# Optimization experiments

Measured on AMD Instinct MI355X. Metric: run time of the kernel, lower is better.

Reference implementation:

```python
import jax, jax.numpy as jnp
import numpy as np


def setup_inputs() -> dict:
    key = jax.random.key(0)
    k1, k2, k3 = jax.random.split(key, 3)
    B, T, J, D = 32, 1024, 128, 256  # D = 2 * input_dim
    ctx_embd = jax.random.normal(k1, (B, T, D), dtype=jnp.float32)
    query_embd = jax.random.normal(k2, (B, J, D), dtype=jnp.float32)
    # nn.Linear(6*input_dim, 1, bias=False) weight flattened: [w1 | w2 | w3], each of size D
    w = jax.random.normal(k3, (3 * D,), dtype=jnp.float32) * (1.0 / np.sqrt(3 * D))
    return {"ctx_embd": ctx_embd, "query_embd": query_embd, "w": w}


def reference(ctx_embd, query_embd, w):
    D = ctx_embd.shape[-1]
    w1, w2, w3 = w[:D], w[D:2 * D], w[2 * D:]
    # Trilinear score S[b,t,j] = ctx.w1 + query.w2 + (ctx*query).w3, decomposed
    # (algebraically identical to Linear(cat(ctx, query, ctx*query))).
    s_ctx = ctx_embd @ w1            # [B, T]
    s_qry = query_embd @ w2          # [B, J]
    s_mul = jnp.einsum('btd,bjd->btj', ctx_embd * w3, query_embd)  # [B, T, J]
    S = s_ctx[:, :, None] + s_qry[:, None, :] + s_mul              # [B, T, J]
    # Context-to-query attention
    a = jax.nn.softmax(S, axis=-1)                                 # [B, T, J]
    c2q = jnp.einsum('btj,bjd->btd', a, query_embd)                # [B, T, D]
    # Query-to-context attention
    b = jax.nn.softmax(jnp.max(S, axis=2), axis=-1)                # [B, T]
    q2c = jnp.einsum('bt,btd->bd', b, ctx_embd)[:, None, :]        # [B, 1, D] broadcast over T
    G = jnp.concatenate(
        [ctx_embd, c2q, ctx_embd * c2q, ctx_embd * q2c], axis=-1)  # [B, T, 4D]
    return G
```

## Files before the change

kernel.cpp:

```cpp
#include <hip/hip_runtime.h>

typedef float f4 __attribute__((ext_vector_type(4)));
typedef short s8v __attribute__((ext_vector_type(8)));
typedef unsigned int u2v __attribute__((ext_vector_type(2)));
typedef unsigned int u4v __attribute__((ext_vector_type(4)));

#define B_ 32
#define T_ 1024
#define J_ 128
#define D_ 256

__device__ inline unsigned short f2bf(float x) {
    unsigned int u = __float_as_uint(x);
    u += 0x7fffu + ((u >> 16) & 1u);
    return (unsigned short)(u >> 16);
}

__device__ __forceinline__ void ldsload16(const void* g, void* l) {
    __builtin_amdgcn_global_load_lds(
        (const __attribute__((address_space(1))) void*)g,
        (__attribute__((address_space(3))) void*)l, 16, 0, 0);
}

__global__ __launch_bounds__(256) void k_pre(const float* __restrict__ q, const float* __restrict__ w,
                                             unsigned short* __restrict__ Bqh, float* __restrict__ sq,
                                             unsigned short* __restrict__ qTh) {
    __shared__ float t_[16][260];
    int b = blockIdx.x >> 3, jt = blockIdx.x & 7;
    int tid = threadIdx.x;
    const float* qb = q + (b * J_ + jt * 16) * D_;

#pragma unroll
    for (int k = 0; k < 4; k++) {
        int idx = tid + (k << 8);
        int jj = idx >> 6, d4 = idx & 63;
        f4 v = *(const f4*)(qb + jj * D_ + (d4 << 2));
        *(f4*)&t_[jj][d4 << 2] = v;
        f4 w1v = *(const f4*)(w + (d4 << 2));
        f4 w3v = *(const f4*)(w + 2 * D_ + (d4 << 2));
        u2v p;
        p[0] = (unsigned int)f2bf(w3v[0] * v[0] + w1v[0]) | ((unsigned int)f2bf(w3v[1] * v[1] + w1v[1]) << 16);
        p[1] = (unsigned int)f2bf(w3v[2] * v[2] + w1v[2]) | ((unsigned int)f2bf(w3v[3] * v[3] + w1v[3]) << 16);
        *(u2v*)(Bqh + (b * J_ + jt * 16 + jj) * D_ + (d4 << 2)) = p;
    }
    __syncthreads();

    {
        int jj = tid >> 4, dg = tid & 15;
        float p = 0.f;
#pragma unroll
        for (int i = 0; i < 16; i++) {
            int d = (dg << 4) + i;
            p += t_[jj][d] * w[D_ + d];
        }
#pragma unroll
        for (int m = 8; m >= 1; m >>= 1) p += __shfl_xor(p, m);
        if (dg == 0) sq[b * J_ + jt * 16 + jj] = p;
    }

    {
        int dd = tid;
        unsigned int pk[8];
#pragma unroll
        for (int i = 0; i < 8; i++) {
            pk[i] = (unsigned int)f2bf(t_[2 * i][dd]) | ((unsigned int)f2bf(t_[2 * i + 1][dd]) << 16);
        }
        u4v v0, v1;
        v0[0] = pk[0]; v0[1] = pk[1]; v0[2] = pk[2]; v0[3] = pk[3];
        v1[0] = pk[4]; v1[1] = pk[5]; v1[2] = pk[6]; v1[3] = pk[7];
        unsigned short* dst = qTh + (b * D_ + dd) * J_ + jt * 16;
        *(u4v*)dst = v0;
        *(u4v*)(dst + 8) = v1;
    }
}

__global__ __launch_bounds__(256, 3) void k_main(const float* __restrict__ ctx,
                                                 const unsigned short* __restrict__ Bqh,
                                                 const unsigned short* __restrict__ qTh,
                                                 const float* __restrict__ sq,
                                                 float* __restrict__ pq2c, float* __restrict__ pms,
                                                 float* __restrict__ out) {
    __shared__ __align__(16) char lds[41600];
    char* B0 = lds;
    char* B1 = lds + 16384;
    char* Ps = lds + 32768;
    float* sc = (float*)(lds + 40960);
    float* mrow = (float*)(lds + 41472);

    int b  = blockIdx.x >> 5;
    int t0 = (blockIdx.x & 31) << 5;
    int tid = threadIdx.x;
    int w = tid >> 6, l = tid & 63, lr = l & 15, lq = l >> 4;
    int rg = w & 1, ch = w >> 1;
    int R0 = rg << 4;

    const unsigned short* BqB  = Bqh + b * J_ * D_;
    const unsigned short* qThB = qTh + b * D_ * J_;

    auto stageBq = [&](char* buf, int qt) {
#pragma unroll
        for (int i = 0; i < 4; i++) {
            int g = tid + (i << 8);
            int jr = g >> 3, c = g & 7;
            ldsload16(BqB + jr * D_ + (qt << 6) + ((c ^ (jr & 7)) << 3),
                      buf + (i << 12) + (w << 10));
        }
    };
    auto stageQ = [&](char* buf, int st) {
#pragma unroll
        for (int i = 0; i < 4; i++) {
            int g = tid + (i << 8);
            int dr = g >> 4, c = g & 15;
            ldsload16(qThB + ((st << 6) + dr) * J_ + ((c ^ (dr & 7)) << 3),
                      buf + (i << 12) + (w << 10));
        }
    };

    f4 acc[4];
#pragma unroll
    for (int nf = 0; nf < 4; nf++) acc[nf] = (f4){0.f, 0.f, 0.f, 0.f};

    stageBq(B0, 0);
    stageBq(B1, 1);

    const float* ctxA = ctx + (b * T_ + t0 + R0 + lr) * D_;
    s8v af[8];
    {
        f4 c0[8], c1[8];
#pragma unroll
        for (int k = 0; k < 8; k++) {
            c0[k] = *(const f4*)(ctxA + k * 32 + lq * 8);
            c1[k] = *(const f4*)(ctxA + k * 32 + lq * 8 + 4);
        }
#pragma unroll
        for (int k = 0; k < 8; k++) {
            union { unsigned short u[8]; s8v v; } t;
#pragma unroll
            for (int e = 0; e < 4; e++) { t.u[e] = f2bf(c0[k][e]); t.u[e + 4] = f2bf(c1[k][e]); }
            af[k] = t.v;
        }
    }

    auto mfmaA = [&](char* buf, int qt) {
#pragma unroll
        for (int kk = 0; kk < 2; kk++)
#pragma unroll
            for (int nf = 0; nf < 4; nf++) {
                int jr = (ch << 6) + (nf << 4) + lr;
                s8v bv = *(const s8v*)(buf + (jr << 7) + ((((kk << 2) | lq) ^ (jr & 7)) << 4));
                acc[nf] = __builtin_amdgcn_mfma_f32_16x16x32_bf16(af[(qt << 1) | kk], bv, acc[nf], 0, 0, 0);
            }
    };

    __syncthreads();
    mfmaA(B0, 0);
    __syncthreads();
    stageBq(B0, 2);
    mfmaA(B1, 1);
    __syncthreads();
    stageBq(B1, 3);
    mfmaA(B0, 2);
    __syncthreads();
    stageQ(B0, 0);
    mfmaA(B1, 3);

    float sqv[4];
#pragma unroll
    for (int nf = 0; nf < 4; nf++) sqv[nf] = sq[b * J_ + (ch << 6) + (nf << 4) + lr];
    float mp[4];
#pragma unroll
    for (int r = 0; r < 4; r++) {
        float m = -1e30f;
#pragma unroll
        for (int nf = 0; nf < 4; nf++) { acc[nf][r] += sqv[nf]; m = fmaxf(m, acc[nf][r]); }
#pragma unroll
        for (int msk = 8; msk >= 1; msk >>= 1) m = fmaxf(m, __shfl_xor(m, msk));
        float s = 0.f;
#pragma unroll
        for (int nf = 0; nf < 4; nf++) { float e = __expf(acc[nf][r] - m); acc[nf][r] = e; s += e; }
#pragma unroll
        for (int msk = 8; msk >= 1; msk >>= 1) s += __shfl_xor(s, msk);
        mp[r] = m;
        if (lr == 0) {
            int row = R0 + (lq << 2) + r;
            sc[(row << 2) + (ch << 1)] = m;
            sc[(row << 2) + (ch << 1) + 1] = s;
        }
    }
    __syncthreads();
    stageQ(B1, 1);

#pragma unroll
    for (int r = 0; r < 4; r++) {
        int row = R0 + (lq << 2) + r;
        float m0 = sc[(row << 2)],     s0 = sc[(row << 2) + 1];
        float m1 = sc[(row << 2) + 2], s1 = sc[(row << 2) + 3];
        float m = fmaxf(m0, m1);
        float sum = s0 * __expf(m0 - m) + s1 * __expf(m1 - m);
        float scale = __expf(mp[r] - m) / sum;
#pragma unroll
        for (int nf = 0; nf < 4; nf++) {
            int cc = (ch << 6) + (nf << 4) + lr;
            int chunk = cc >> 3;
            *(unsigned short*)(Ps + row * 256 + ((chunk ^ (row & 7)) << 4) + ((lr & 7) << 1)) =
                f2bf(acc[nf][r] * scale);
        }
        if (ch == 0 && lr == 0) mrow[row] = m;
    }
    __syncthreads();

    int dh2 = w >> 1;
    int prow = R0 + lr;
    s8v pf[4];
#pragma unroll
    for (int jk = 0; jk < 4; jk++)
        pf[jk] = *(const s8v*)(Ps + prow * 256 + ((((jk << 2) + lq) ^ (prow & 7)) << 4));

    f4 acc2[8];
#pragma unroll
    for (int ai = 0; ai < 8; ai++) acc2[ai] = (f4){0.f, 0.f, 0.f, 0.f};

    auto mfmaB = [&](char* rb, int s) {
#pragma unroll
        for (int df2 = 0; df2 < 2; df2++) {
            int dr = (dh2 << 5) + (df2 << 4) + lr;
            int ai = (s << 1) + df2;
#pragma unroll
            for (int jk = 0; jk < 4; jk++) {
                s8v bv = *(const s8v*)(rb + (dr << 8) + ((((jk << 2) + lq) ^ (dr & 7)) << 4));
                acc2[ai] = __builtin_amdgcn_mfma_f32_16x16x32_bf16(pf[jk], bv, acc2[ai], 0, 0, 0);
            }
        }
    };

    mfmaB(B0, 0);
    __syncthreads();
    stageQ(B0, 2);
    mfmaB(B1, 1);
    __syncthreads();
    stageQ(B1, 3);
    mfmaB(B0, 2);
    __syncthreads();
    mfmaB(B1, 3);
    __syncthreads();

    float* cq = (float*)lds;
#pragma unroll
    for (int s2 = 0; s2 < 4; s2++)
#pragma unroll
        for (int df2 = 0; df2 < 2; df2++) {
            int col = (s2 << 6) + (dh2 << 5) + (df2 << 4) + lr;
            int ai = (s2 << 1) + df2;
            int chunk = col >> 2;
#pragma unroll
            for (int r = 0; r < 4; r++) {
                int row = R0 + (lq << 2) + r;
                *(float*)((char*)cq + (row << 10) + ((chunk ^ (row & 7)) << 4) + ((col & 3) << 2)) = acc2[ai][r];
            }
        }
    __syncthreads();

    {
        int row = tid >> 3;
        int o = b * T_ + t0 + row;
        const float* crow = ctx + o * D_;
        float* orow = out + o * 1024;
#pragma unroll
        for (int i = 0; i < 8; i++) {
            int col4 = (i << 5) + ((tid & 7) << 2);
            int chunk = col4 >> 2;
            f4 val = *(const f4*)((char*)cq + (row << 10) + ((chunk ^ (row & 7)) << 4));
            f4 cx = *(const f4*)(crow + col4);
            f4 v3 = cx * val;
            __builtin_nontemporal_store(cx, (f4*)(orow + col4));
            __builtin_nontemporal_store(val, (f4*)(orow + 256 + col4));
            __builtin_nontemporal_store(v3, (f4*)(orow + 512 + col4));
        }
    }

    {
        float mblk = -1e30f;
#pragma unroll 8
        for (int t = 0; t < 32; t++) mblk = fmaxf(mblk, mrow[t]);
        float sblk = 0.f, q2a = 0.f;
        const float* cpart = ctx + (b * T_ + t0) * D_ + tid;
#pragma unroll 4
        for (int t = 0; t < 32; t++) {
            float e = __expf(mrow[t] - mblk);
            sblk += e;
            q2a += e * cpart[t * D_];
        }
        pq2c[blockIdx.x * 256 + tid] = q2a;
        if (tid == 0) { pms[blockIdx.x * 2] = mblk; pms[blockIdx.x * 2 + 1] = sblk; }
    }
}

__global__ __launch_bounds__(256) void k_tail(const float* __restrict__ ctx,
                                              const float* __restrict__ pq2c, const float* __restrict__ pms,
                                              float* __restrict__ out) {
    int b = blockIdx.x >> 5, tc = blockIdx.x & 31;
    int tid = threadIdx.x;
    const float* pm = pms + b * 64;

    float mx = -1e30f;
#pragma unroll 8
    for (int i = 0; i < 32; i++) mx = fmaxf(mx, pm[2 * i]);
    float sm = 0.f, q2 = 0.f;
#pragma unroll 4
    for (int i = 0; i < 32; i++) {
        float e = __expf(pm[2 * i] - mx);
        sm += pm[2 * i + 1] * e;
        q2 += e * pq2c[((b << 5) + i) * 256 + tid];
    }
    q2 /= sm;
    __shared__ float q2s[256];
    q2s[tid] = q2;
    __syncthreads();

    int row = tid >> 3;
    int o = b * T_ + tc * 32 + row;
    const float* crow = ctx + o * D_;
    float* orow = out + o * 1024;
#pragma unroll
    for (int i = 0; i < 8; i++) {
        int col4 = (i << 5) + ((tid & 7) << 2);
        f4 cx = *(const f4*)(crow + col4);
        f4 qv = *(const f4*)&q2s[col4];
        f4 r = cx * qv;
        __builtin_nontemporal_store(r, (f4*)(orow + 768 + col4));
    }
}

extern "C" void kernel_launch(void* const* d_in, const int* in_sizes, int n_in,
                              void* d_out, int out_size, void* d_ws, size_t ws_size,
                              hipStream_t stream) {
    const float* ctx   = (const float*)d_in[0];
    const float* query = (const float*)d_in[1];
    const float* w     = (const float*)d_in[2];
    float* out = (float*)d_out;

    unsigned short* Bqh = (unsigned short*)d_ws;
    unsigned short* qTh = Bqh + B_ * J_ * D_;
    float* fws = (float*)(qTh + B_ * J_ * D_);
    float* sq   = fws;
    float* pq2c = fws + 4096;
    float* pms  = fws + 4096 + 1024 * 256;

    k_pre<<<B_ * 8, 256, 0, stream>>>(query, w, Bqh, sq, qTh);
    k_main<<<B_ * (T_ / 32), 256, 0, stream>>>(ctx, Bqh, qTh, sq, pq2c, pms, out);
    k_tail<<<B_ * 32, 256, 0, stream>>>(ctx, pq2c, pms, out);
}
```

Baseline: 70.17 us.

## Raise k_main occupancy, shrink LDS, remap blocks, split q2c partials per wave pair

Occupancy is raised from 3 to 4 blocks per CU by trimming LDS to 40960 bytes: the softmax scratch now reuses the B1 buffer, and the mrow array is dropped in favour of register shuffles. The block-to-batch mapping is permuted so consecutive blocks touch different batches. The q2c partial reduction now runs per 16-row group with vectorized f2 loads, doubling the partials that k_tail must merge. The stageQ prefetch into B1 moves later to avoid clobbering the scratch, which cuts overlap, and the tighter register budget may cause spills.

After: 66.74 us. 4.9% less time.

```diff
diff --git a/kernel.cpp b/kernel.cpp
--- a/kernel.cpp
+++ b/kernel.cpp
@@ -1,6 +1,7 @@
 #include <hip/hip_runtime.h>
 
 typedef float f4 __attribute__((ext_vector_type(4)));
+typedef float f2 __attribute__((ext_vector_type(2)));
 typedef short s8v __attribute__((ext_vector_type(8)));
 typedef unsigned int u2v __attribute__((ext_vector_type(2)));
 typedef unsigned int u4v __attribute__((ext_vector_type(4)));
@@ -74,21 +75,22 @@
     }
 }
 
-__global__ __launch_bounds__(256, 3) void k_main(const float* __restrict__ ctx,
+__global__ __launch_bounds__(256, 4) void k_main(const float* __restrict__ ctx,
                                                  const unsigned short* __restrict__ Bqh,
                                                  const unsigned short* __restrict__ qTh,
                                                  const float* __restrict__ sq,
                                                  float* __restrict__ pq2c, float* __restrict__ pms,
                                                  float* __restrict__ out) {
-    __shared__ __align__(16) char lds[41600];
+    __shared__ __align__(16) char lds[40960];
     char* B0 = lds;
     char* B1 = lds + 16384;
     char* Ps = lds + 32768;
-    float* sc = (float*)(lds + 40960);
-    float* mrow = (float*)(lds + 41472);
-
-    int b  = blockIdx.x >> 5;
-    int t0 = (blockIdx.x & 31) << 5;
+    float* sc = (float*)B1;
+
+    int bid = blockIdx.x;
+    int b  = ((bid & 7) << 2) | ((bid >> 3) & 3);
+    int tc = bid >> 5;
+    int t0 = tc << 5;
     int tid = threadIdx.x;
     int w = tid >> 6, l = tid & 63, lr = l & 15, lq = l >> 4;
     int rg = w & 1, ch = w >> 1;
@@ -125,20 +127,14 @@
 
     const float* ctxA = ctx + (b * T_ + t0 + R0 + lr) * D_;
     s8v af[8];
-    {
-        f4 c0[8], c1[8];
-#pragma unroll
-        for (int k = 0; k < 8; k++) {
-            c0[k] = *(const f4*)(ctxA + k * 32 + lq * 8);
-            c1[k] = *(const f4*)(ctxA + k * 32 + lq * 8 + 4);
-        }
-#pragma unroll
-        for (int k = 0; k < 8; k++) {
-            union { unsigned short u[8]; s8v v; } t;
-#pragma unroll
-            for (int e = 0; e < 4; e++) { t.u[e] = f2bf(c0[k][e]); t.u[e + 4] = f2bf(c1[k][e]); }
-            af[k] = t.v;
-        }
+#pragma unroll
+    for (int k = 0; k < 8; k++) {
+        f4 a0 = *(const f4*)(ctxA + k * 32 + lq * 8);
+        f4 a1 = *(const f4*)(ctxA + k * 32 + lq * 8 + 4);
+        union { unsigned short u[8]; s8v v; } t;
+#pragma unroll
+        for (int e = 0; e < 4; e++) { t.u[e] = f2bf(a0[e]); t.u[e + 4] = f2bf(a1[e]); }
+        af[k] = t.v;
     }
 
     auto mfmaA = [&](char* buf, int qt) {
@@ -167,7 +163,7 @@
     float sqv[4];
 #pragma unroll
     for (int nf = 0; nf < 4; nf++) sqv[nf] = sq[b * J_ + (ch << 6) + (nf << 4) + lr];
-    float mp[4];
+    float mp[4], sp[4];
 #pragma unroll
     for (int r = 0; r < 4; r++) {
         float m = -1e30f;
@@ -180,16 +176,20 @@
         for (int nf = 0; nf < 4; nf++) { float e = __expf(acc[nf][r] - m); acc[nf][r] = e; s += e; }
 #pragma unroll
         for (int msk = 8; msk >= 1; msk >>= 1) s += __shfl_xor(s, msk);
-        mp[r] = m;
-        if (lr == 0) {
+        mp[r] = m; sp[r] = s;
+    }
+    __syncthreads();
+    if (lr == 0) {
+#pragma unroll
+        for (int r = 0; r < 4; r++) {
             int row = R0 + (lq << 2) + r;
-            sc[(row << 2) + (ch << 1)] = m;
-            sc[(row << 2) + (ch << 1) + 1] = s;
-        }
-    }
-    __syncthreads();
-    stageQ(B1, 1);
-
+            sc[(row << 2) + (ch << 1)] = mp[r];
+            sc[(row << 2) + (ch << 1) + 1] = sp[r];
+        }
+    }
+    __syncthreads();
+
+    float mm[4];
 #pragma unroll
     for (int r = 0; r < 4; r++) {
         int row = R0 + (lq << 2) + r;
@@ -205,11 +205,11 @@
             *(unsigned short*)(Ps + row * 256 + ((chunk ^ (row & 7)) << 4) + ((lr & 7) << 1)) =
                 f2bf(acc[nf][r] * scale);
         }
-        if (ch == 0 && lr == 0) mrow[row] = m;
-    }
-    __syncthreads();
-
-    int dh2 = w >> 1;
+        mm[r] = m;
+    }
+    __syncthreads();
+    stageQ(B1, 1);
+
     int prow = R0 + lr;
     s8v pf[4];
 #pragma unroll
@@ -223,7 +223,7 @@
     auto mfmaB = [&](char* rb, int s) {
 #pragma unroll
         for (int df2 = 0; df2 < 2; df2++) {
-            int dr = (dh2 << 5) + (df2 << 4) + lr;
+            int dr = (ch << 5) + (df2 << 4) + lr;
             int ai = (s << 1) + df2;
 #pragma unroll
             for (int jk = 0; jk < 4; jk++) {
@@ -249,7 +249,7 @@
     for (int s2 = 0; s2 < 4; s2++)
 #pragma unroll
         for (int df2 = 0; df2 < 2; df2++) {
-            int col = (s2 << 6) + (dh2 << 5) + (df2 << 4) + lr;
+            int col = (s2 << 6) + (ch << 5) + (df2 << 4) + lr;
             int ai = (s2 << 1) + df2;
             int chunk = col >> 2;
 #pragma unroll
@@ -279,19 +279,25 @@
     }
 
     {
-        float mblk = -1e30f;
-#pragma unroll 8
-        for (int t = 0; t < 32; t++) mblk = fmaxf(mblk, mrow[t]);
-        float sblk = 0.f, q2a = 0.f;
-        const float* cpart = ctx + (b * T_ + t0) * D_ + tid;
+        float m16[16];
+#pragma unroll
+        for (int i = 0; i < 16; i++) m16[i] = __shfl(mm[i & 3], (i >> 2) << 4);
+        float mw = -1e30f;
+#pragma unroll
+        for (int i = 0; i < 16; i++) mw = fmaxf(mw, m16[i]);
+        const float* cp = ctx + (b * T_ + t0 + R0) * D_ + (ch << 7) + (l << 1);
+        f2 p = (f2){0.f, 0.f};
+        float sw_ = 0.f;
 #pragma unroll 4
-        for (int t = 0; t < 32; t++) {
-            float e = __expf(mrow[t] - mblk);
-            sblk += e;
-            q2a += e * cpart[t * D_];
-        }
-        pq2c[blockIdx.x * 256 + tid] = q2a;
-        if (tid == 0) { pms[blockIdx.x * 2] = mblk; pms[blockIdx.x * 2 + 1] = sblk; }
+        for (int t = 0; t < 16; t++) {
+            float e = __expf(m16[t] - mw);
+            sw_ += e;
+            f2 cv = *(const f2*)(cp + t * D_);
+            p.x += e * cv.x; p.y += e * cv.y;
+        }
+        int pidx = (((b << 5) | tc) << 1) | rg;
+        *(f2*)(pq2c + (pidx << 8) + (ch << 7) + (l << 1)) = p;
+        if (ch == 0 && l == 0) { pms[pidx * 2] = mw; pms[pidx * 2 + 1] = sw_; }
     }
 }
 
@@ -300,17 +306,17 @@
                                               float* __restrict__ out) {
     int b = blockIdx.x >> 5, tc = blockIdx.x & 31;
     int tid = threadIdx.x;
-    const float* pm = pms + b * 64;
+    const float* pm = pms + b * 128;
 
     float mx = -1e30f;
 #pragma unroll 8
-    for (int i = 0; i < 32; i++) mx = fmaxf(mx, pm[2 * i]);
+    for (int i = 0; i < 64; i++) mx = fmaxf(mx, pm[2 * i]);
     float sm = 0.f, q2 = 0.f;
 #pragma unroll 4
-    for (int i = 0; i < 32; i++) {
+    for (int i = 0; i < 64; i++) {
         float e = __expf(pm[2 * i] - mx);
         sm += pm[2 * i + 1] * e;
-        q2 += e * pq2c[((b << 5) + i) * 256 + tid];
+        q2 += e * pq2c[((b << 6) + i) * 256 + tid];
     }
     q2 /= sm;
     __shared__ float q2s[256];
@@ -344,7 +350,7 @@
     float* fws = (float*)(qTh + B_ * J_ * D_);
     float* sq   = fws;
     float* pq2c = fws + 4096;
-    float* pms  = fws + 4096 + 1024 * 256;
+    float* pms  = fws + 4096 + 2048 * 256;
 
     k_pre<<<B_ * 8, 256, 0, stream>>>(query, w, Bqh, sq, qTh);
     k_main<<<B_ * (T_ / 32), 256, 0, stream>>>(ctx, Bqh, qTh, sq, pq2c, pms, out);
```
